# Kernel tuning notes

Hardware: AMD Instinct MI355X
Metric: run time of the kernel (lower is better)

The kernel has to match this reference:

```python
import jax, jax.numpy as jnp
import numpy as np

B, S, D = 4, 2048, 1024  # batch, seq_len, d_model


def setup_inputs() -> dict:
    key = jax.random.key(0)
    k0, k1, k2, k3 = jax.random.split(key, 4)
    x = jax.random.normal(k0, (B, S, D), dtype=jnp.float32)
    W_Q = jax.random.normal(k1, (D, D), dtype=jnp.float32) * (D ** -0.5)
    W_K = jax.random.normal(k2, (D, D), dtype=jnp.float32) * (D ** -0.5)
    W_V = jax.random.normal(k3, (D, D), dtype=jnp.float32) * (D ** -0.5)
    return {"x": x, "W_Q": W_Q, "W_K": W_K, "W_V": W_V}


def reference(x, W_Q, W_K, W_V):
    # Q/K/V projections: input @ W.t()
    Q = jnp.matmul(x, W_Q.T)  # [B,S,D]
    K = jnp.matmul(x, W_K.T)  # [B,S,D]
    V = jnp.matmul(x, W_V.T)  # [B,S,D]
    b, s, d = K.shape
    # Faithful to original: a row-major RESHAPE of K (not a transpose!)
    K_r = K.reshape(b, d, s)  # [B,D,S]
    scores = jnp.matmul(Q, K_r) / d  # divided by d_model (not sqrt), per source
    attn = jax.nn.softmax(scores, axis=-1)  # [B,S,S]
    return jnp.matmul(attn, V)  # [B,S,D]
```

## Files before the change

kernel.cpp:

```cpp
#include <hip/hip_runtime.h>
#include <hip/hip_bf16.h>
#include <stdint.h>

#define BB 4
#define SS 2048
#define DD 1024

typedef __attribute__((ext_vector_type(4))) float f32x4;
typedef __attribute__((ext_vector_type(8))) __bf16 bf16x8;

typedef const __attribute__((address_space(1))) void* gptr_t;
typedef __attribute__((address_space(3))) void* lptr_t;

__device__ __forceinline__ void load_lds16(const void* g, void* l) {
  __builtin_amdgcn_global_load_lds((gptr_t)g, (lptr_t)l, 16, 0, 0);
}

#define SBAR0() __builtin_amdgcn_sched_barrier(0)

template <int N>
__device__ __forceinline__ void wait_vmcnt() {
  if constexpr (N == 0) asm volatile("s_waitcnt vmcnt(0)" ::: "memory");
  else if constexpr (N == 6) asm volatile("s_waitcnt vmcnt(6)" ::: "memory");
  else if constexpr (N == 8) asm volatile("s_waitcnt vmcnt(8)" ::: "memory");
}
__device__ __forceinline__ void wait_lgkm0() {
  asm volatile("s_waitcnt lgkmcnt(0)" ::: "memory");
}

__device__ __forceinline__ unsigned short f2bf(float x) {
  union { float f; uint32_t u; } v; v.f = x;
  uint32_t u = v.u;
  return (unsigned short)((u + 0x7FFFu + ((u >> 16) & 1u)) >> 16);
}
__device__ __forceinline__ float bf2f(unsigned short h) {
  union { uint32_t u; float f; } v; v.u = ((uint32_t)h) << 16; return v.f;
}

__global__ __launch_bounds__(256) void convert_x(
    const float* __restrict__ in, unsigned short* __restrict__ out, int n4) {
  for (int i = blockIdx.x * 256 + threadIdx.x; i < n4; i += gridDim.x * 256) {
    float4 v = ((const float4*)in)[i];
    ushort4 o;
    o.x = f2bf(v.x); o.y = f2bf(v.y); o.z = f2bf(v.z); o.w = f2bf(v.w);
    ((ushort4*)out)[i] = o;
  }
}

__global__ __launch_bounds__(256) void convert_w(
    const float* __restrict__ wq, const float* __restrict__ wk,
    const float* __restrict__ wv, unsigned short* __restrict__ wcat) {
  const int n4 = DD * DD / 4;
  int i = blockIdx.x * 256 + threadIdx.x;
  const int which = i / n4, j = i - which * n4;
  const float* src = (which == 0) ? wq : ((which == 1) ? wk : wv);
  float4 v = ((const float4*)src)[j];
  ushort4 o;
  o.x = f2bf(v.x); o.y = f2bf(v.y); o.z = f2bf(v.z); o.w = f2bf(v.w);
  ((ushort4*)(wcat + (size_t)which * DD * DD))[j] = o;
}

template <int BM, int KLEN>
__device__ __forceinline__ void gemm_core(
    const unsigned short* __restrict__ A, const unsigned short* __restrict__ Bt,
    int lda, int ldb, int row0, int col0, char* lds,
    f32x4 (&acc)[BM / 32][4]) {
  constexpr int M_REP = BM / 32;
  constexpr int NT   = KLEN / 64;
  constexpr int ASZ  = BM * 128;
  constexpr int BUFSZ = ASZ + 32768;
  constexpr int LPT  = (BM + 256) / 64;
  constexpr int NA   = BM / 64;

  const int tid  = threadIdx.x;
  const int lane = tid & 63;
  const int w    = tid >> 6;
  const int wr = w >> 2, wc = w & 3;

#pragma unroll
  for (int f = 0; f < M_REP; ++f)
#pragma unroll
    for (int n = 0; n < 4; ++n) acc[f][n] = (f32x4)(0.f);

  const int l8 = lane >> 3, l7 = lane & 7;
  const int swz = l7 ^ l8;
  const unsigned short* srcA = A  + (size_t)(row0 + w * (BM / 8) + l8) * lda + swz * 8;
  const unsigned short* srcB = Bt + (size_t)(col0 + w * 32 + l8) * ldb + swz * 8;
  char* ldsAw = lds + w * (BM / 8) * 128;
  char* ldsBw = lds + ASZ + w * 4096;

  const int l15 = lane & 15, l16 = lane >> 4;
  const int xc0 = ((l16) ^ l7) * 16;
  const int xc1 = ((4 + l16) ^ l7) * 16;
  const char* rdA = lds + wr * (BM / 2) * 128 + l15 * 128;
  const char* rdB = lds + ASZ + wc * 8192 + l15 * 128;

  auto STAGE = [&](int kt) {
    const unsigned short* a = srcA + kt * 64;
    const unsigned short* b = srcB + kt * 64;
    char* la = ldsAw + (kt & 1) * BUFSZ;
    char* lb = ldsBw + (kt & 1) * BUFSZ;
#pragma unroll
    for (int c = 0; c < NA; ++c) load_lds16(a + (size_t)c * 8 * lda, la + c * 1024);
#pragma unroll
    for (int c = 0; c < 4; ++c)  load_lds16(b + (size_t)c * 8 * ldb, lb + c * 1024);
  };

  STAGE(0);
  STAGE(1);

#pragma unroll 1
  for (int t = 0; t < NT; ++t) {
    if (t == NT - 1) wait_vmcnt<0>(); else wait_vmcnt<LPT>();
    SBAR0();
    __builtin_amdgcn_s_barrier();
    SBAR0();

    const char* pA = rdA + (t & 1) * BUFSZ;
    const char* pB = rdB + (t & 1) * BUFSZ;

    bf16x8 a0[M_REP], b0[4], a1[M_REP], b1[4];
#pragma unroll
    for (int n = 0; n < 4; ++n) b0[n] = *(const bf16x8*)(pB + xc0 + n * 2048);
#pragma unroll
    for (int f = 0; f < M_REP; ++f) a0[f] = *(const bf16x8*)(pA + xc0 + f * 2048);

    __builtin_amdgcn_s_setprio(1);
#pragma unroll
    for (int f = 0; f < M_REP; ++f)
#pragma unroll
      for (int n = 0; n < 4; ++n)
        acc[f][n] = __builtin_amdgcn_mfma_f32_16x16x32_bf16(a0[f], b0[n], acc[f][n], 0, 0, 0);
    __builtin_amdgcn_s_setprio(0);

#pragma unroll
    for (int n = 0; n < 4; ++n) b1[n] = *(const bf16x8*)(pB + xc1 + n * 2048);
#pragma unroll
    for (int f = 0; f < M_REP; ++f) a1[f] = *(const bf16x8*)(pA + xc1 + f * 2048);

    wait_lgkm0();
    SBAR0();
    __builtin_amdgcn_s_barrier();
    SBAR0();
    if (t + 2 < NT) STAGE(t + 2);

    __builtin_amdgcn_s_setprio(1);
#pragma unroll
    for (int f = 0; f < M_REP; ++f)
#pragma unroll
      for (int n = 0; n < 4; ++n)
        acc[f][n] = __builtin_amdgcn_mfma_f32_16x16x32_bf16(a1[f], b1[n], acc[f][n], 0, 0, 0);
    __builtin_amdgcn_s_setprio(0);
  }
}

__global__ __launch_bounds__(512, 2) void proj_gemm(
    const unsigned short* __restrict__ xb, const unsigned short* __restrict__ wcat,
    unsigned short* __restrict__ q, unsigned short* __restrict__ kk,
    unsigned short* __restrict__ vv) {
  extern __shared__ char lds[];
  f32x4 acc[4][4];
  const int bn = blockIdx.x, bm = blockIdx.y;
  gemm_core<128, 1024>(xb, wcat, 1024, 1024, bm * 128, bn * 256, lds, acc);

  const int lane = threadIdx.x & 63, w = threadIdx.x >> 6;
  const int wr = w >> 2, wc = w & 3;
  const int which = bn >> 2;
  unsigned short* dst = (which == 0) ? q : ((which == 1) ? kk : vv);
  const int colb = (bn & 3) * 256 + wc * 64 + (lane & 15);
  const int rowb = bm * 128 + wr * 64 + (lane >> 4) * 4;
#pragma unroll
  for (int f = 0; f < 4; ++f)
#pragma unroll
    for (int i = 0; i < 4; ++i) {
      const size_t rowoff = (size_t)(rowb + f * 16 + i) * 1024;
#pragma unroll
      for (int n = 0; n < 4; ++n)
        dst[rowoff + colb + n * 16] = f2bf(acc[f][n][i]);
    }
}

__global__ __launch_bounds__(256) void k_to_mt(
    const unsigned short* __restrict__ k, unsigned short* __restrict__ mt) {
  const int z = blockIdx.z, b = z >> 1, delta = z & 1;
  const unsigned short* kb = k + (size_t)b * SS * DD + (size_t)delta * DD;
  unsigned short* mtb = mt + (size_t)b * SS * DD + (size_t)delta * DD * DD;
  __shared__ unsigned short tile[32][33];
  const int tx = threadIdx.x, ty = threadIdx.y;
  const int i0 = blockIdx.x * 32, j0 = blockIdx.y * 32;
#pragma unroll
  for (int yy = ty; yy < 32; yy += 8)
    tile[yy][tx] = kb[(size_t)(i0 + yy) * 2048 + j0 + tx];
  __syncthreads();
#pragma unroll
  for (int yy = ty; yy < 32; yy += 8)
    mtb[(size_t)(j0 + yy) * 1024 + i0 + tx] = tile[tx][yy];
}

__global__ __launch_bounds__(256) void v_to_vt(
    const unsigned short* __restrict__ v, unsigned short* __restrict__ vt) {
  const int b = blockIdx.z;
  const unsigned short* vb = v + (size_t)b * SS * DD;
  unsigned short* vtb = vt + (size_t)b * DD * SS;
  __shared__ unsigned short tile[32][33];
  const int tx = threadIdx.x, ty = threadIdx.y;
  const int k0 = blockIdx.x * 32, n0 = blockIdx.y * 32;
#pragma unroll
  for (int yy = ty; yy < 32; yy += 8)
    tile[yy][tx] = vb[(size_t)(k0 + yy) * 1024 + n0 + tx];
  __syncthreads();
#pragma unroll
  for (int yy = ty; yy < 32; yy += 8)
    vtb[(size_t)(n0 + yy) * 2048 + k0 + tx] = tile[tx][yy];
}

__global__ __launch_bounds__(512, 2) void score_gemm(
    const unsigned short* __restrict__ q, const unsigned short* __restrict__ mt,
    unsigned short* __restrict__ sc) {
  extern __shared__ char lds[];
  f32x4 acc[8][4];
  const int b = blockIdx.z;
  gemm_core<256, 1024>(q + (size_t)b * SS * DD, mt + (size_t)b * SS * DD,
                       1024, 1024, blockIdx.y * 256, blockIdx.x * 256, lds, acc);
  unsigned short* out = sc + (size_t)b * SS * SS;
  const int lane = threadIdx.x & 63, w = threadIdx.x >> 6;
  const int wr = w >> 2, wc = w & 3;
  const int colb = blockIdx.x * 256 + wc * 64 + (lane & 15);
  const int rowb = blockIdx.y * 256 + wr * 128 + (lane >> 4) * 4;
  const float scale = 1.0f / 1024.0f;
#pragma unroll
  for (int f = 0; f < 8; ++f)
#pragma unroll
    for (int i = 0; i < 4; ++i) {
      const size_t rowoff = (size_t)(rowb + f * 16 + i) * 2048;
#pragma unroll
      for (int n = 0; n < 4; ++n)
        out[rowoff + colb + n * 16] = f2bf(acc[f][n][i] * scale);
    }
}

__global__ __launch_bounds__(256) void softmax_kernel(unsigned short* __restrict__ sc) {
  const size_t row = blockIdx.x;
  unsigned short* io = sc + row * 2048;
  const int t = threadIdx.x;
  ushort4 u0 = ((const ushort4*)io)[t];
  ushort4 u1 = ((const ushort4*)io)[t + 256];
  float v[8];
  v[0] = bf2f(u0.x); v[1] = bf2f(u0.y); v[2] = bf2f(u0.z); v[3] = bf2f(u0.w);
  v[4] = bf2f(u1.x); v[5] = bf2f(u1.y); v[6] = bf2f(u1.z); v[7] = bf2f(u1.w);
  float m = v[0];
#pragma unroll
  for (int j = 1; j < 8; ++j) m = fmaxf(m, v[j]);
#pragma unroll
  for (int off = 32; off > 0; off >>= 1) m = fmaxf(m, __shfl_xor(m, off));
  __shared__ float redm[4], reds[4];
  const int w = t >> 6;
  if ((t & 63) == 0) redm[w] = m;
  __syncthreads();
  m = fmaxf(fmaxf(redm[0], redm[1]), fmaxf(redm[2], redm[3]));
  float s = 0.f;
#pragma unroll
  for (int j = 0; j < 8; ++j) { v[j] = __expf(v[j] - m); s += v[j]; }
#pragma unroll
  for (int off = 32; off > 0; off >>= 1) s += __shfl_xor(s, off);
  if ((t & 63) == 0) reds[w] = s;
  __syncthreads();
  const float inv = 1.0f / (reds[0] + reds[1] + reds[2] + reds[3]);
  ushort4 o0, o1;
  o0.x = f2bf(v[0] * inv); o0.y = f2bf(v[1] * inv); o0.z = f2bf(v[2] * inv); o0.w = f2bf(v[3] * inv);
  o1.x = f2bf(v[4] * inv); o1.y = f2bf(v[5] * inv); o1.z = f2bf(v[6] * inv); o1.w = f2bf(v[7] * inv);
  ((ushort4*)io)[t] = o0;
  ((ushort4*)io)[t + 256] = o1;
}

__global__ __launch_bounds__(512, 2) void pv_gemm(
    const unsigned short* __restrict__ p, const unsigned short* __restrict__ vt,
    float* __restrict__ out) {
  extern __shared__ char lds[];
  f32x4 acc[4][4];
  const int b = blockIdx.z;
  gemm_core<128, 2048>(p + (size_t)b * SS * SS, vt + (size_t)b * DD * SS,
                       2048, 2048, blockIdx.y * 128, blockIdx.x * 256, lds, acc);
  float* ob = out + (size_t)b * SS * DD;
  const int lane = threadIdx.x & 63, w = threadIdx.x >> 6;
  const int wr = w >> 2, wc = w & 3;
  const int colb = blockIdx.x * 256 + wc * 64 + (lane & 15);
  const int rowb = blockIdx.y * 128 + wr * 64 + (lane >> 4) * 4;
#pragma unroll
  for (int f = 0; f < 4; ++f)
#pragma unroll
    for (int i = 0; i < 4; ++i) {
      const size_t rowoff = (size_t)(rowb + f * 16 + i) * 1024;
#pragma unroll
      for (int n = 0; n < 4; ++n)
        ob[rowoff + colb + n * 16] = acc[f][n][i];
    }
}

extern "C" void kernel_launch(void* const* d_in, const int* in_sizes, int n_in,
                              void* d_out, int out_size, void* d_ws, size_t ws_size,
                              hipStream_t stream) {
  const float* x  = (const float*)d_in[0];
  const float* wq = (const float*)d_in[1];
  const float* wk = (const float*)d_in[2];
  const float* wv = (const float*)d_in[3];
  float* out = (float*)d_out;
  uint8_t* ws = (uint8_t*)d_ws;

  const size_t MB = 1u << 20;
  unsigned short* xb   = (unsigned short*)(ws);
  unsigned short* wcat = (unsigned short*)(ws + 16 * MB);
  unsigned short* q    = (unsigned short*)(ws + 22 * MB);
  unsigned short* kk   = (unsigned short*)(ws + 38 * MB);
  unsigned short* vv   = (unsigned short*)(ws + 54 * MB);
  unsigned short* mt   = (unsigned short*)(ws + 70 * MB);
  unsigned short* vt   = (unsigned short*)(ws + 86 * MB);
  unsigned short* sc   = (unsigned short*)(ws + 102 * MB);

  convert_x<<<2048, 256, 0, stream>>>(x, xb, BB * SS * DD / 4);
  convert_w<<<3 * DD * DD / 4 / 256, 256, 0, stream>>>(wq, wk, wv, wcat);
  proj_gemm<<<dim3(12, 64), 512, 96 * 1024, stream>>>(xb, wcat, q, kk, vv);
  k_to_mt<<<dim3(32, 32, 8), dim3(32, 8), 0, stream>>>(kk, mt);
  v_to_vt<<<dim3(64, 32, 4), dim3(32, 8), 0, stream>>>(vv, vt);
  score_gemm<<<dim3(8, 8, 4), 512, 128 * 1024, stream>>>(q, mt, sc);
  softmax_kernel<<<BB * SS, 256, 0, stream>>>(sc);
  pv_gemm<<<dim3(4, 16, 4), 512, 96 * 1024, stream>>>(sc, vt, out);
}
```

Measured before the change: 265.2 us.

## Restructure GEMM core into four-stage LDS pipeline with 32-wide K steps

Replaces the double-buffered 64-wide K tile loop in the shared GEMM core with a four-buffer ring of 32-wide K tiles, prefetching three stages ahead. It drops one of the two block barriers per iteration and issues the next stage's global-to-LDS loads between the LDS reads and the MFMAs. The LDS layout and XOR swizzle change to 64-byte rows. The aim is to hide global load latency better and cut synchronisation, at the cost of more iterations, a different LDS footprint, and possible new bank conflicts.

```diff
diff --git a/kernel.cpp b/kernel.cpp
--- a/kernel.cpp
+++ b/kernel.cpp
@@ -21,6 +21,8 @@
 template <int N>
 __device__ __forceinline__ void wait_vmcnt() {
   if constexpr (N == 0) asm volatile("s_waitcnt vmcnt(0)" ::: "memory");
+  else if constexpr (N == 3) asm volatile("s_waitcnt vmcnt(3)" ::: "memory");
+  else if constexpr (N == 4) asm volatile("s_waitcnt vmcnt(4)" ::: "memory");
   else if constexpr (N == 6) asm volatile("s_waitcnt vmcnt(6)" ::: "memory");
   else if constexpr (N == 8) asm volatile("s_waitcnt vmcnt(8)" ::: "memory");
 }
@@ -66,91 +68,94 @@
     int lda, int ldb, int row0, int col0, char* lds,
     f32x4 (&acc)[BM / 32][4]) {
   constexpr int M_REP = BM / 32;
-  constexpr int NT   = KLEN / 64;
-  constexpr int ASZ  = BM * 128;
-  constexpr int BUFSZ = ASZ + 32768;
-  constexpr int LPT  = (BM + 256) / 64;
-  constexpr int NA   = BM / 64;
-
-  const int tid  = threadIdx.x;
-  const int lane = tid & 63;
-  const int w    = tid >> 6;
+  constexpr int NT   = KLEN / 32;
+  constexpr int RA   = BM / 128;
+  constexpr int LPS  = RA + 2;
+  constexpr int ASUB = BM * 64;
+  constexpr int BSUB = 16384;
+
+  const int tid = threadIdx.x, lane = tid & 63, w = tid >> 6;
   const int wr = w >> 2, wc = w & 3;
 
 #pragma unroll
-  for (int f = 0; f < M_REP; ++f)
-#pragma unroll
-    for (int n = 0; n < 4; ++n) acc[f][n] = (f32x4)(0.f);
-
-  const int l8 = lane >> 3, l7 = lane & 7;
-  const int swz = l7 ^ l8;
-  const unsigned short* srcA = A  + (size_t)(row0 + w * (BM / 8) + l8) * lda + swz * 8;
-  const unsigned short* srcB = Bt + (size_t)(col0 + w * 32 + l8) * ldb + swz * 8;
-  char* ldsAw = lds + w * (BM / 8) * 128;
-  char* ldsBw = lds + ASZ + w * 4096;
-
-  const int l15 = lane & 15, l16 = lane >> 4;
-  const int xc0 = ((l16) ^ l7) * 16;
-  const int xc1 = ((4 + l16) ^ l7) * 16;
-  const char* rdA = lds + wr * (BM / 2) * 128 + l15 * 128;
-  const char* rdB = lds + ASZ + wc * 8192 + l15 * 128;
-
-  auto STAGE = [&](int kt) {
-    const unsigned short* a = srcA + kt * 64;
-    const unsigned short* b = srcB + kt * 64;
-    char* la = ldsAw + (kt & 1) * BUFSZ;
-    char* lb = ldsBw + (kt & 1) * BUFSZ;
-#pragma unroll
-    for (int c = 0; c < NA; ++c) load_lds16(a + (size_t)c * 8 * lda, la + c * 1024);
-#pragma unroll
-    for (int c = 0; c < 4; ++c)  load_lds16(b + (size_t)c * 8 * ldb, lb + c * 1024);
+  for (int m = 0; m < M_REP; ++m)
+#pragma unroll
+    for (int n = 0; n < 4; ++n) acc[m][n] = (f32x4)(0.f);
+
+  const int arow = tid >> 2;
+  const int acol = (tid & 3) ^ ((tid >> 2) & 3);
+  const unsigned short* srcA = A  + (size_t)(row0 + arow) * lda + acol * 8;
+  const unsigned short* srcB = Bt + (size_t)(col0 + arow) * ldb + acol * 8;
+
+  const int xcol = ((lane >> 4) ^ (lane & 3)) * 16;
+  const char* rdA = lds + (wr * (BM / 2) + (lane & 15)) * 64 + xcol;
+  const char* rdB = lds + 4 * ASUB + (wc * 64 + (lane & 15)) * 64 + xcol;
+
+  auto STAGE_A = [&](int k) {
+    char* d = lds + (k & 3) * ASUB + w * 1024;
+    const unsigned short* s = srcA + k * 32;
+#pragma unroll
+    for (int r = 0; r < RA; ++r)
+      load_lds16(s + (size_t)r * 128 * lda, d + r * 8192);
   };
-
-  STAGE(0);
-  STAGE(1);
+  auto STAGE_B = [&](int k) {
+    char* d = lds + 4 * ASUB + (k & 3) * BSUB + w * 1024;
+    const unsigned short* s = srcB + k * 32;
+#pragma unroll
+    for (int r = 0; r < 2; ++r)
+      load_lds16(s + (size_t)r * 128 * ldb, d + r * 8192);
+  };
+
+  STAGE_A(0); STAGE_B(0);
+  STAGE_A(1); STAGE_B(1);
+  STAGE_A(2); STAGE_B(2);
 
 #pragma unroll 1
-  for (int t = 0; t < NT; ++t) {
-    if (t == NT - 1) wait_vmcnt<0>(); else wait_vmcnt<LPT>();
+  for (int k = 0; k < NT; ++k) {
+    if (k + 2 < NT) wait_vmcnt<2 * LPS>();
+    else if (k + 1 < NT) wait_vmcnt<LPS>();
+    else wait_vmcnt<0>();
     SBAR0();
     __builtin_amdgcn_s_barrier();
     SBAR0();
 
-    const char* pA = rdA + (t & 1) * BUFSZ;
-    const char* pB = rdB + (t & 1) * BUFSZ;
-
-    bf16x8 a0[M_REP], b0[4], a1[M_REP], b1[4];
-#pragma unroll
-    for (int n = 0; n < 4; ++n) b0[n] = *(const bf16x8*)(pB + xc0 + n * 2048);
-#pragma unroll
-    for (int f = 0; f < M_REP; ++f) a0[f] = *(const bf16x8*)(pA + xc0 + f * 2048);
-
-    __builtin_amdgcn_s_setprio(1);
-#pragma unroll
-    for (int f = 0; f < M_REP; ++f)
-#pragma unroll
-      for (int n = 0; n < 4; ++n)
-        acc[f][n] = __builtin_amdgcn_mfma_f32_16x16x32_bf16(a0[f], b0[n], acc[f][n], 0, 0, 0);
-    __builtin_amdgcn_s_setprio(0);
-
-#pragma unroll
-    for (int n = 0; n < 4; ++n) b1[n] = *(const bf16x8*)(pB + xc1 + n * 2048);
-#pragma unroll
-    for (int f = 0; f < M_REP; ++f) a1[f] = *(const bf16x8*)(pA + xc1 + f * 2048);
-
+    const char* pA = rdA + (k & 3) * ASUB;
+    const char* pB = rdB + (k & 3) * BSUB;
+
+    bf16x8 bf[4], af[4];
+#pragma unroll
+    for (int n = 0; n < 4; ++n) bf[n] = *(const bf16x8*)(pB + n * 1024);
+#pragma unroll
+    for (int m = 0; m < 4; ++m) af[m] = *(const bf16x8*)(pA + m * 1024);
+    if (k + 3 < NT) {
+      STAGE_A(k + 3);
+      if constexpr (M_REP == 4) STAGE_B(k + 3);
+    }
     wait_lgkm0();
     SBAR0();
-    __builtin_amdgcn_s_barrier();
-    SBAR0();
-    if (t + 2 < NT) STAGE(t + 2);
-
     __builtin_amdgcn_s_setprio(1);
 #pragma unroll
-    for (int f = 0; f < M_REP; ++f)
+    for (int m = 0; m < 4; ++m)
 #pragma unroll
       for (int n = 0; n < 4; ++n)
-        acc[f][n] = __builtin_amdgcn_mfma_f32_16x16x32_bf16(a1[f], b1[n], acc[f][n], 0, 0, 0);
+        acc[m][n] = __builtin_amdgcn_mfma_f32_16x16x32_bf16(af[m], bf[n], acc[m][n], 0, 0, 0);
     __builtin_amdgcn_s_setprio(0);
+
+    if constexpr (M_REP == 8) {
+      bf16x8 ag[4];
+#pragma unroll
+      for (int m = 0; m < 4; ++m) ag[m] = *(const bf16x8*)(pA + (4 + m) * 1024);
+      if (k + 3 < NT) STAGE_B(k + 3);
+      wait_lgkm0();
+      SBAR0();
+      __builtin_amdgcn_s_setprio(1);
+#pragma unroll
+      for (int m = 0; m < 4; ++m)
+#pragma unroll
+        for (int n = 0; n < 4; ++n)
+          acc[4 + m][n] = __builtin_amdgcn_mfma_f32_16x16x32_bf16(ag[m], bf[n], acc[4 + m][n], 0, 0, 0);
+      __builtin_amdgcn_s_setprio(0);
+    }
   }
 }
 
```

Measured after the change: 275.0 us. 1.04x slower.

## Restructure GEMM core into issue-then-barrier 8-wave schedule with single prefetch

Applied to the files above, without the earlier changes.

Rewrites the shared GEMM main loop. Each iteration now issues the next tile's global-to-LDS loads right after the first fragment reads, in place of keeping two stages in flight. The loop waits on vmcnt(0) every iteration and inserts extra workgroup barriers around each MFMA cluster, so the waves run in lockstep. The global load mapping also changes so each wave loads interleaved 8-row chunks strided by 64 rows. This trades prefetch depth for a tighter, barrier-synchronised interleave of LDS reads and MFMA. The risk is exposed memory latency and added barrier overhead.

```diff
diff --git a/kernel.cpp b/kernel.cpp
--- a/kernel.cpp
+++ b/kernel.cpp
@@ -18,11 +18,8 @@
 
 #define SBAR0() __builtin_amdgcn_sched_barrier(0)
 
-template <int N>
-__device__ __forceinline__ void wait_vmcnt() {
-  if constexpr (N == 0) asm volatile("s_waitcnt vmcnt(0)" ::: "memory");
-  else if constexpr (N == 6) asm volatile("s_waitcnt vmcnt(6)" ::: "memory");
-  else if constexpr (N == 8) asm volatile("s_waitcnt vmcnt(8)" ::: "memory");
+__device__ __forceinline__ void wait_vm0() {
+  asm volatile("s_waitcnt vmcnt(0)" ::: "memory");
 }
 __device__ __forceinline__ void wait_lgkm0() {
   asm volatile("s_waitcnt lgkmcnt(0)" ::: "memory");
@@ -61,96 +58,123 @@
 }
 
 template <int BM, int KLEN>
-__device__ __forceinline__ void gemm_core(
+__device__ __forceinline__ void gemm_core8(
     const unsigned short* __restrict__ A, const unsigned short* __restrict__ Bt,
     int lda, int ldb, int row0, int col0, char* lds,
     f32x4 (&acc)[BM / 32][4]) {
   constexpr int M_REP = BM / 32;
   constexpr int NT   = KLEN / 64;
   constexpr int ASZ  = BM * 128;
-  constexpr int BUFSZ = ASZ + 32768;
-  constexpr int LPT  = (BM + 256) / 64;
-  constexpr int NA   = BM / 64;
-
-  const int tid  = threadIdx.x;
-  const int lane = tid & 63;
-  const int w    = tid >> 6;
+  constexpr int BUF  = ASZ + 32768;
+  constexpr int NCA  = BM / 64;
+
+  const int tid = threadIdx.x, lane = tid & 63, w = tid >> 6;
   const int wr = w >> 2, wc = w & 3;
-
-#pragma unroll
-  for (int f = 0; f < M_REP; ++f)
-#pragma unroll
-    for (int n = 0; n < 4; ++n) acc[f][n] = (f32x4)(0.f);
-
-  const int l8 = lane >> 3, l7 = lane & 7;
-  const int swz = l7 ^ l8;
-  const unsigned short* srcA = A  + (size_t)(row0 + w * (BM / 8) + l8) * lda + swz * 8;
-  const unsigned short* srcB = Bt + (size_t)(col0 + w * 32 + l8) * ldb + swz * 8;
-  char* ldsAw = lds + w * (BM / 8) * 128;
-  char* ldsBw = lds + ASZ + w * 4096;
-
-  const int l15 = lane & 15, l16 = lane >> 4;
-  const int xc0 = ((l16) ^ l7) * 16;
+  const int l8 = lane >> 3, l7 = lane & 7, l15 = lane & 15, l16 = lane >> 4;
+
+#pragma unroll
+  for (int m = 0; m < M_REP; ++m)
+#pragma unroll
+    for (int n = 0; n < 4; ++n) acc[m][n] = (f32x4)(0.f);
+
+  const unsigned short* srcA = A  + (size_t)(row0 + w * 8 + l8) * lda + (l7 ^ l8) * 8;
+  const unsigned short* srcB = Bt + (size_t)(col0 + w * 8 + l8) * ldb + (l7 ^ l8) * 8;
+
+  const int xc0 = (l16 ^ l7) * 16;
   const int xc1 = ((4 + l16) ^ l7) * 16;
-  const char* rdA = lds + wr * (BM / 2) * 128 + l15 * 128;
-  const char* rdB = lds + ASZ + wc * 8192 + l15 * 128;
-
-  auto STAGE = [&](int kt) {
-    const unsigned short* a = srcA + kt * 64;
-    const unsigned short* b = srcB + kt * 64;
-    char* la = ldsAw + (kt & 1) * BUFSZ;
-    char* lb = ldsBw + (kt & 1) * BUFSZ;
-#pragma unroll
-    for (int c = 0; c < NA; ++c) load_lds16(a + (size_t)c * 8 * lda, la + c * 1024);
-#pragma unroll
-    for (int c = 0; c < 4; ++c)  load_lds16(b + (size_t)c * 8 * ldb, lb + c * 1024);
+  const int rdAo = (wr * (BM / 2) + l15) * 128;
+  const int rdBo = ASZ + (wc * 64 + l15) * 128;
+
+  auto STAGE = [&](int t) {
+    char* ab = lds + (t & 1) * BUF + w * 1024;
+    char* bb = lds + (t & 1) * BUF + ASZ + w * 1024;
+    const unsigned short* a = srcA + t * 64;
+    const unsigned short* b = srcB + t * 64;
+#pragma unroll
+    for (int j = 0; j < NCA; ++j) load_lds16(a + (size_t)j * 64 * lda, ab + j * 8192);
+#pragma unroll
+    for (int j = 0; j < 4; ++j)  load_lds16(b + (size_t)j * 64 * ldb, bb + j * 8192);
   };
 
   STAGE(0);
-  STAGE(1);
 
 #pragma unroll 1
   for (int t = 0; t < NT; ++t) {
-    if (t == NT - 1) wait_vmcnt<0>(); else wait_vmcnt<LPT>();
+    wait_vm0();
     SBAR0();
     __builtin_amdgcn_s_barrier();
     SBAR0();
-
-    const char* pA = rdA + (t & 1) * BUFSZ;
-    const char* pB = rdB + (t & 1) * BUFSZ;
-
-    bf16x8 a0[M_REP], b0[4], a1[M_REP], b1[4];
-#pragma unroll
-    for (int n = 0; n < 4; ++n) b0[n] = *(const bf16x8*)(pB + xc0 + n * 2048);
-#pragma unroll
-    for (int f = 0; f < M_REP; ++f) a0[f] = *(const bf16x8*)(pA + xc0 + f * 2048);
-
+    const char* pA = lds + (t & 1) * BUF + rdAo;
+    const char* pB = lds + (t & 1) * BUF + rdBo;
+
+    bf16x8 bfr[4], afr[4];
+#pragma unroll
+    for (int n = 0; n < 4; ++n) bfr[n] = *(const bf16x8*)(pB + xc0 + n * 2048);
+#pragma unroll
+    for (int m = 0; m < 4; ++m) afr[m] = *(const bf16x8*)(pA + xc0 + m * 2048);
+    if (t + 1 < NT) STAGE(t + 1);
+    SBAR0();
+    __builtin_amdgcn_s_barrier();
+    wait_lgkm0();
+    SBAR0();
     __builtin_amdgcn_s_setprio(1);
 #pragma unroll
-    for (int f = 0; f < M_REP; ++f)
-#pragma unroll
-      for (int n = 0; n < 4; ++n)
-        acc[f][n] = __builtin_amdgcn_mfma_f32_16x16x32_bf16(a0[f], b0[n], acc[f][n], 0, 0, 0);
+    for (int m = 0; m < 4; ++m)
+#pragma unroll
+      for (int n = 0; n < 4; ++n)
+        acc[m][n] = __builtin_amdgcn_mfma_f32_16x16x32_bf16(afr[m], bfr[n], acc[m][n], 0, 0, 0);
     __builtin_amdgcn_s_setprio(0);
-
-#pragma unroll
-    for (int n = 0; n < 4; ++n) b1[n] = *(const bf16x8*)(pB + xc1 + n * 2048);
-#pragma unroll
-    for (int f = 0; f < M_REP; ++f) a1[f] = *(const bf16x8*)(pA + xc1 + f * 2048);
-
+    __builtin_amdgcn_s_barrier();
+
+    if constexpr (M_REP == 8) {
+#pragma unroll
+      for (int m = 0; m < 4; ++m) afr[m] = *(const bf16x8*)(pA + xc0 + (4 + m) * 2048);
+      SBAR0();
+      __builtin_amdgcn_s_barrier();
+      wait_lgkm0();
+      SBAR0();
+      __builtin_amdgcn_s_setprio(1);
+#pragma unroll
+      for (int m = 0; m < 4; ++m)
+#pragma unroll
+        for (int n = 0; n < 4; ++n)
+          acc[4 + m][n] = __builtin_amdgcn_mfma_f32_16x16x32_bf16(afr[m], bfr[n], acc[4 + m][n], 0, 0, 0);
+      __builtin_amdgcn_s_setprio(0);
+      __builtin_amdgcn_s_barrier();
+    }
+
+#pragma unroll
+    for (int n = 0; n < 4; ++n) bfr[n] = *(const bf16x8*)(pB + xc1 + n * 2048);
+#pragma unroll
+    for (int m = 0; m < 4; ++m) afr[m] = *(const bf16x8*)(pA + xc1 + m * 2048);
+    SBAR0();
+    __builtin_amdgcn_s_barrier();
     wait_lgkm0();
     SBAR0();
-    __builtin_amdgcn_s_barrier();
-    SBAR0();
-    if (t + 2 < NT) STAGE(t + 2);
-
     __builtin_amdgcn_s_setprio(1);
 #pragma unroll
-    for (int f = 0; f < M_REP; ++f)
-#pragma unroll
-      for (int n = 0; n < 4; ++n)
-        acc[f][n] = __builtin_amdgcn_mfma_f32_16x16x32_bf16(a1[f], b1[n], acc[f][n], 0, 0, 0);
+    for (int m = 0; m < 4; ++m)
+#pragma unroll
+      for (int n = 0; n < 4; ++n)
+        acc[m][n] = __builtin_amdgcn_mfma_f32_16x16x32_bf16(afr[m], bfr[n], acc[m][n], 0, 0, 0);
     __builtin_amdgcn_s_setprio(0);
+
+    if constexpr (M_REP == 8) {
+      __builtin_amdgcn_s_barrier();
+#pragma unroll
+      for (int m = 0; m < 4; ++m) afr[m] = *(const bf16x8*)(pA + xc1 + (4 + m) * 2048);
+      SBAR0();
+      __builtin_amdgcn_s_barrier();
+      wait_lgkm0();
+      SBAR0();
+      __builtin_amdgcn_s_setprio(1);
+#pragma unroll
+      for (int m = 0; m < 4; ++m)
+#pragma unroll
+        for (int n = 0; n < 4; ++n)
+          acc[4 + m][n] = __builtin_amdgcn_mfma_f32_16x16x32_bf16(afr[m], bfr[n], acc[4 + m][n], 0, 0, 0);
+      __builtin_amdgcn_s_setprio(0);
+    }
   }
 }
 
@@ -161,7 +185,7 @@
   extern __shared__ char lds[];
   f32x4 acc[4][4];
   const int bn = blockIdx.x, bm = blockIdx.y;
-  gemm_core<128, 1024>(xb, wcat, 1024, 1024, bm * 128, bn * 256, lds, acc);
+  gemm_core8<128, 1024>(xb, wcat, 1024, 1024, bm * 128, bn * 256, lds, acc);
 
   const int lane = threadIdx.x & 63, w = threadIdx.x >> 6;
   const int wr = w >> 2, wc = w & 3;
@@ -220,8 +244,8 @@
   extern __shared__ char lds[];
   f32x4 acc[8][4];
   const int b = blockIdx.z;
-  gemm_core<256, 1024>(q + (size_t)b * SS * DD, mt + (size_t)b * SS * DD,
-                       1024, 1024, blockIdx.y * 256, blockIdx.x * 256, lds, acc);
+  gemm_core8<256, 1024>(q + (size_t)b * SS * DD, mt + (size_t)b * SS * DD,
+                        1024, 1024, blockIdx.y * 256, blockIdx.x * 256, lds, acc);
   unsigned short* out = sc + (size_t)b * SS * SS;
   const int lane = threadIdx.x & 63, w = threadIdx.x >> 6;
   const int wr = w >> 2, wc = w & 3;
@@ -279,8 +303,8 @@
   extern __shared__ char lds[];
   f32x4 acc[4][4];
   const int b = blockIdx.z;
-  gemm_core<128, 2048>(p + (size_t)b * SS * SS, vt + (size_t)b * DD * SS,
-                       2048, 2048, blockIdx.y * 128, blockIdx.x * 256, lds, acc);
+  gemm_core8<128, 2048>(p + (size_t)b * SS * SS, vt + (size_t)b * DD * SS,
+                        2048, 2048, blockIdx.y * 128, blockIdx.x * 256, lds, acc);
   float* ob = out + (size_t)b * SS * DD;
   const int lane = threadIdx.x & 63, w = threadIdx.x >> 6;
   const int wr = w >> 2, wc = w & 3;
```

Measured after the change: 264.7 us. About the same (-0.2%).

## Restructure GEMM core to single-stage prefetch with phased fragment loads and larger proj tile

Applied to the files above, without the earlier changes.

Replaces the two-stage-ahead prefetch GEMM core with a version that issues the next K-tile's global-to-LDS loads right after the barrier, waits on vmcnt(0) every iteration, and interleaves LDS fragment loads with MFMA in phases of two M-fragments, preloading both K-halves of B. It also changes the cooperative load mapping to whole-block row striping, and raises the projection GEMM tile from 128 to 256 rows with 128KB LDS. The aim is fewer barriers per iteration and more reuse per block, at the cost of less prefetch depth, so load latency may be exposed. With 128KB LDS and launch bounds of 2 blocks, occupancy may also drop.

```diff
diff --git a/kernel.cpp b/kernel.cpp
--- a/kernel.cpp
+++ b/kernel.cpp
@@ -18,11 +18,8 @@
 
 #define SBAR0() __builtin_amdgcn_sched_barrier(0)
 
-template <int N>
-__device__ __forceinline__ void wait_vmcnt() {
-  if constexpr (N == 0) asm volatile("s_waitcnt vmcnt(0)" ::: "memory");
-  else if constexpr (N == 6) asm volatile("s_waitcnt vmcnt(6)" ::: "memory");
-  else if constexpr (N == 8) asm volatile("s_waitcnt vmcnt(8)" ::: "memory");
+__device__ __forceinline__ void wait_vm0() {
+  asm volatile("s_waitcnt vmcnt(0)" ::: "memory");
 }
 __device__ __forceinline__ void wait_lgkm0() {
   asm volatile("s_waitcnt lgkmcnt(0)" ::: "memory");
@@ -61,96 +58,93 @@
 }
 
 template <int BM, int KLEN>
-__device__ __forceinline__ void gemm_core(
+__device__ __forceinline__ void gemm_coreF(
     const unsigned short* __restrict__ A, const unsigned short* __restrict__ Bt,
     int lda, int ldb, int row0, int col0, char* lds,
     f32x4 (&acc)[BM / 32][4]) {
   constexpr int M_REP = BM / 32;
+  constexpr int NPH  = M_REP / 2;
   constexpr int NT   = KLEN / 64;
+  constexpr int NCA  = BM / 64;
   constexpr int ASZ  = BM * 128;
-  constexpr int BUFSZ = ASZ + 32768;
-  constexpr int LPT  = (BM + 256) / 64;
-  constexpr int NA   = BM / 64;
-
-  const int tid  = threadIdx.x;
-  const int lane = tid & 63;
-  const int w    = tid >> 6;
+  constexpr int BUF  = ASZ + 32768;
+
+  const int tid = threadIdx.x, lane = tid & 63, w = tid >> 6;
   const int wr = w >> 2, wc = w & 3;
-
-#pragma unroll
-  for (int f = 0; f < M_REP; ++f)
-#pragma unroll
-    for (int n = 0; n < 4; ++n) acc[f][n] = (f32x4)(0.f);
-
-  const int l8 = lane >> 3, l7 = lane & 7;
-  const int swz = l7 ^ l8;
-  const unsigned short* srcA = A  + (size_t)(row0 + w * (BM / 8) + l8) * lda + swz * 8;
-  const unsigned short* srcB = Bt + (size_t)(col0 + w * 32 + l8) * ldb + swz * 8;
-  char* ldsAw = lds + w * (BM / 8) * 128;
-  char* ldsBw = lds + ASZ + w * 4096;
-
-  const int l15 = lane & 15, l16 = lane >> 4;
-  const int xc0 = ((l16) ^ l7) * 16;
+  const int l7 = lane & 7, l15 = lane & 15, l16 = lane >> 4;
+
+#pragma unroll
+  for (int m = 0; m < M_REP; ++m)
+#pragma unroll
+    for (int n = 0; n < 4; ++n) acc[m][n] = (f32x4)(0.f);
+
+  const int srow = tid >> 3;
+  const int scol = (tid & 7) ^ (srow & 7);
+  const unsigned short* sA = A  + (size_t)(row0 + srow) * lda + scol * 8;
+  const unsigned short* sB = Bt + (size_t)(col0 + srow) * ldb + scol * 8;
+
+  auto SA = [&](int t, int c) {
+    load_lds16(sA + (size_t)c * 64 * lda + t * 64, lds + (t & 1) * BUF + c * 8192 + tid * 16);
+  };
+  auto SB = [&](int t, int c) {
+    load_lds16(sB + (size_t)c * 64 * ldb + t * 64, lds + (t & 1) * BUF + ASZ + c * 8192 + tid * 16);
+  };
+
+  const int xc0 = (l16 ^ l7) * 16;
   const int xc1 = ((4 + l16) ^ l7) * 16;
-  const char* rdA = lds + wr * (BM / 2) * 128 + l15 * 128;
-  const char* rdB = lds + ASZ + wc * 8192 + l15 * 128;
-
-  auto STAGE = [&](int kt) {
-    const unsigned short* a = srcA + kt * 64;
-    const unsigned short* b = srcB + kt * 64;
-    char* la = ldsAw + (kt & 1) * BUFSZ;
-    char* lb = ldsBw + (kt & 1) * BUFSZ;
-#pragma unroll
-    for (int c = 0; c < NA; ++c) load_lds16(a + (size_t)c * 8 * lda, la + c * 1024);
-#pragma unroll
-    for (int c = 0; c < 4; ++c)  load_lds16(b + (size_t)c * 8 * ldb, lb + c * 1024);
-  };
-
-  STAGE(0);
-  STAGE(1);
+  const char* rA = lds + (wr * (BM / 2) + l15) * 128;
+  const char* rB = lds + ASZ + (wc * 64 + l15) * 128;
+
+#pragma unroll
+  for (int c = 0; c < NCA; ++c) SA(0, c);
+#pragma unroll
+  for (int c = 0; c < 4; ++c) SB(0, c);
 
 #pragma unroll 1
   for (int t = 0; t < NT; ++t) {
-    if (t == NT - 1) wait_vmcnt<0>(); else wait_vmcnt<LPT>();
+    wait_vm0();
     SBAR0();
     __builtin_amdgcn_s_barrier();
     SBAR0();
-
-    const char* pA = rdA + (t & 1) * BUFSZ;
-    const char* pB = rdB + (t & 1) * BUFSZ;
-
-    bf16x8 a0[M_REP], b0[4], a1[M_REP], b1[4];
-#pragma unroll
-    for (int n = 0; n < 4; ++n) b0[n] = *(const bf16x8*)(pB + xc0 + n * 2048);
-#pragma unroll
-    for (int f = 0; f < M_REP; ++f) a0[f] = *(const bf16x8*)(pA + xc0 + f * 2048);
-
-    __builtin_amdgcn_s_setprio(1);
-#pragma unroll
-    for (int f = 0; f < M_REP; ++f)
-#pragma unroll
-      for (int n = 0; n < 4; ++n)
-        acc[f][n] = __builtin_amdgcn_mfma_f32_16x16x32_bf16(a0[f], b0[n], acc[f][n], 0, 0, 0);
-    __builtin_amdgcn_s_setprio(0);
-
-#pragma unroll
-    for (int n = 0; n < 4; ++n) b1[n] = *(const bf16x8*)(pB + xc1 + n * 2048);
-#pragma unroll
-    for (int f = 0; f < M_REP; ++f) a1[f] = *(const bf16x8*)(pA + xc1 + f * 2048);
-
-    wait_lgkm0();
+    if (t + 1 < NT) {
+#pragma unroll
+      for (int c = 0; c < NCA; ++c) SA(t + 1, c);
+#pragma unroll
+      for (int c = 0; c < 4; ++c) SB(t + 1, c);
+    }
     SBAR0();
-    __builtin_amdgcn_s_barrier();
-    SBAR0();
-    if (t + 2 < NT) STAGE(t + 2);
-
-    __builtin_amdgcn_s_setprio(1);
-#pragma unroll
-    for (int f = 0; f < M_REP; ++f)
-#pragma unroll
-      for (int n = 0; n < 4; ++n)
-        acc[f][n] = __builtin_amdgcn_mfma_f32_16x16x32_bf16(a1[f], b1[n], acc[f][n], 0, 0, 0);
-    __builtin_amdgcn_s_setprio(0);
+
+    const char* pA = rA + (t & 1) * BUF;
+    const char* pB = rB + (t & 1) * BUF;
+
+    bf16x8 bfr[4][2];
+#pragma unroll
+    for (int n = 0; n < 4; ++n) {
+      bfr[n][0] = *(const bf16x8*)(pB + n * 2048 + xc0);
+      bfr[n][1] = *(const bf16x8*)(pB + n * 2048 + xc1);
+    }
+
+#pragma unroll
+    for (int q = 0; q < NPH; ++q) {
+      bf16x8 af[2][2];
+#pragma unroll
+      for (int i = 0; i < 2; ++i) {
+        af[i][0] = *(const bf16x8*)(pA + (2 * q + i) * 2048 + xc0);
+        af[i][1] = *(const bf16x8*)(pA + (2 * q + i) * 2048 + xc1);
+      }
+      wait_lgkm0();
+      SBAR0();
+      __builtin_amdgcn_s_setprio(1);
+#pragma unroll
+      for (int i = 0; i < 2; ++i)
+#pragma unroll
+        for (int n = 0; n < 4; ++n)
+#pragma unroll
+          for (int ks = 0; ks < 2; ++ks)
+            acc[2 * q + i][n] =
+                __builtin_amdgcn_mfma_f32_16x16x32_bf16(af[i][ks], bfr[n][ks], acc[2 * q + i][n], 0, 0, 0);
+      __builtin_amdgcn_s_setprio(0);
+    }
   }
 }
 
@@ -159,18 +153,18 @@
     unsigned short* __restrict__ q, unsigned short* __restrict__ kk,
     unsigned short* __restrict__ vv) {
   extern __shared__ char lds[];
-  f32x4 acc[4][4];
+  f32x4 acc[8][4];
   const int bn = blockIdx.x, bm = blockIdx.y;
-  gemm_core<128, 1024>(xb, wcat, 1024, 1024, bm * 128, bn * 256, lds, acc);
+  gemm_coreF<256, 1024>(xb, wcat, 1024, 1024, bm * 256, bn * 256, lds, acc);
 
   const int lane = threadIdx.x & 63, w = threadIdx.x >> 6;
   const int wr = w >> 2, wc = w & 3;
   const int which = bn >> 2;
   unsigned short* dst = (which == 0) ? q : ((which == 1) ? kk : vv);
   const int colb = (bn & 3) * 256 + wc * 64 + (lane & 15);
-  const int rowb = bm * 128 + wr * 64 + (lane >> 4) * 4;
-#pragma unroll
-  for (int f = 0; f < 4; ++f)
+  const int rowb = bm * 256 + wr * 128 + (lane >> 4) * 4;
+#pragma unroll
+  for (int f = 0; f < 8; ++f)
 #pragma unroll
     for (int i = 0; i < 4; ++i) {
       const size_t rowoff = (size_t)(rowb + f * 16 + i) * 1024;
@@ -220,8 +214,8 @@
   extern __shared__ char lds[];
   f32x4 acc[8][4];
   const int b = blockIdx.z;
-  gemm_core<256, 1024>(q + (size_t)b * SS * DD, mt + (size_t)b * SS * DD,
-                       1024, 1024, blockIdx.y * 256, blockIdx.x * 256, lds, acc);
+  gemm_coreF<256, 1024>(q + (size_t)b * SS * DD, mt + (size_t)b * SS * DD,
+                        1024, 1024, blockIdx.y * 256, blockIdx.x * 256, lds, acc);
   unsigned short* out = sc + (size_t)b * SS * SS;
   const int lane = threadIdx.x & 63, w = threadIdx.x >> 6;
   const int wr = w >> 2, wc = w & 3;
@@ -279,8 +273,8 @@
   extern __shared__ char lds[];
   f32x4 acc[4][4];
   const int b = blockIdx.z;
-  gemm_core<128, 2048>(p + (size_t)b * SS * SS, vt + (size_t)b * DD * SS,
-                       2048, 2048, blockIdx.y * 128, blockIdx.x * 256, lds, acc);
+  gemm_coreF<128, 2048>(p + (size_t)b * SS * SS, vt + (size_t)b * DD * SS,
+                        2048, 2048, blockIdx.y * 128, blockIdx.x * 256, lds, acc);
   float* ob = out + (size_t)b * SS * DD;
   const int lane = threadIdx.x & 63, w = threadIdx.x >> 6;
   const int wr = w >> 2, wc = w & 3;
@@ -319,7 +313,7 @@
 
   convert_x<<<2048, 256, 0, stream>>>(x, xb, BB * SS * DD / 4);
   convert_w<<<3 * DD * DD / 4 / 256, 256, 0, stream>>>(wq, wk, wv, wcat);
-  proj_gemm<<<dim3(12, 64), 512, 96 * 1024, stream>>>(xb, wcat, q, kk, vv);
+  proj_gemm<<<dim3(12, 32), 512, 128 * 1024, stream>>>(xb, wcat, q, kk, vv);
   k_to_mt<<<dim3(32, 32, 8), dim3(32, 8), 0, stream>>>(kk, mt);
   v_to_vt<<<dim3(64, 32, 4), dim3(32, 8), 0, stream>>>(vv, vt);
   score_gemm<<<dim3(8, 8, 4), 512, 128 * 1024, stream>>>(q, mt, sc);
```

Measured after the change: 263.1 us. About the same (-0.8%).
